# Kernel optimization log

Measured on AMD Instinct MI355X. Metric: run time of the kernel, lower is better.

Reference implementation:

```python
import jax, jax.numpy as jnp
import numpy as np

N, E, IN, HID, H, L, G = 20000, 320000, 128, 64, 4, 3, 128

def setup_inputs() -> dict:
    key = jax.random.key(0)
    ks = jax.random.split(key, 14)
    x = jax.random.normal(ks[0], (N, IN), dtype=jnp.float32)
    edge_index = jax.random.randint(ks[1], (2, E), 0, N, dtype=jnp.int64)
    batch = jnp.sort(jax.random.randint(ks[2], (N,), 0, G, dtype=jnp.int64))
    s_in = 1.0 / np.sqrt(IN)
    s_h = 1.0 / np.sqrt(HID)
    lin_W = jax.random.normal(ks[3], (IN, HID), jnp.float32) * s_in
    lin_b = jax.random.normal(ks[4], (HID,), jnp.float32) * 0.02
    Wq = jax.random.normal(ks[5], (L, HID, H * HID), jnp.float32) * s_h
    bq = jax.random.normal(ks[6], (L, H * HID), jnp.float32) * 0.02
    Wk = jax.random.normal(ks[7], (L, HID, H * HID), jnp.float32) * s_h
    bk = jax.random.normal(ks[8], (L, H * HID), jnp.float32) * 0.02
    Wv = jax.random.normal(ks[9], (L, HID, H * HID), jnp.float32) * s_h
    bv = jax.random.normal(ks[10], (L, H * HID), jnp.float32) * 0.02
    Ws = jax.random.normal(ks[11], (L, HID, HID), jnp.float32) * s_h
    bs = jax.random.normal(ks[12], (L, HID), jnp.float32) * 0.02
    return {"x": x, "edge_index": edge_index, "batch": batch,
            "lin_W": lin_W, "lin_b": lin_b, "Wq": Wq, "bq": bq,
            "Wk": Wk, "bk": bk, "Wv": Wv, "bv": bv, "Ws": Ws, "bs": bs}

def _transformer_conv(h, src, dst, Wq, bq, Wk, bk, Wv, bv, Ws, bs):
    # PyG TransformerConv(hid, hid, heads=H, concat=False), beta=False, root_weight=True
    n = h.shape[0]
    C = HID  # per-head dim
    q = (h @ Wq + bq).reshape(n, H, C)
    k = (h @ Wk + bk).reshape(n, H, C)
    v = (h @ Wv + bv).reshape(n, H, C)
    # per-edge attention logits: q_i . k_j / sqrt(C), i=dst (target), j=src
    alpha = jnp.einsum('ehc,ehc->eh', q[dst], k[src]) * (1.0 / np.sqrt(C))  # [E,H]
    # segment softmax over edges grouped by target node
    amax = jax.ops.segment_max(alpha, dst, num_segments=n)  # [N,H]
    amax = jnp.where(jnp.isfinite(amax), amax, 0.0)
    ex = jnp.exp(alpha - amax[dst])
    denom = jax.ops.segment_sum(ex, dst, num_segments=n)
    a = ex / jnp.maximum(denom[dst], 1e-16)  # [E,H]
    msg = a[:, :, None] * v[src]  # [E,H,C]
    agg = jax.ops.segment_sum(msg.reshape(-1, H * C), dst, num_segments=n)
    out = agg.reshape(n, H, C).mean(axis=1)  # concat=False -> head mean
    return out + h @ Ws + bs  # root/skip connection

def reference(x, edge_index, batch, lin_W, lin_b, Wq, bq, Wk, bk, Wv, bv, Ws, bs):
    src, dst = edge_index[0], edge_index[1]
    h = x @ lin_W + lin_b  # [N, HID]; dropout inactive in eval
    for l in range(L):
        h = jax.nn.relu(_transformer_conv(h, src, dst, Wq[l], bq[l], Wk[l], bk[l],
                                          Wv[l], bv[l], Ws[l], bs[l]))
    # global_add_pool: sum node features per graph
    return jax.ops.segment_sum(h, batch, num_segments=G)  # [G, HID]
```

## Files before the change

kernel.cpp:

```cpp
#include <hip/hip_runtime.h>
#include <math.h>

#define N_NODES 20000
#define N_EDGES 320000
#define DIM_IN 128
#define HID 64
#define HEADS 4
#define LAYERS 3
#define GRAPHS 128
#define HOP 68

typedef unsigned short ushort;
typedef ushort ushort8 __attribute__((ext_vector_type(8)));
typedef ushort ushort4v __attribute__((ext_vector_type(4)));
typedef short short8 __attribute__((ext_vector_type(8)));
typedef float f32x4 __attribute__((ext_vector_type(4)));

__device__ __forceinline__ float bf2f(ushort u) {
    return __uint_as_float(((unsigned int)u) << 16);
}
__device__ __forceinline__ ushort f2bf(float f) {
    unsigned int b = __float_as_uint(f);
    return (ushort)((b + 0x7FFFu + ((b >> 16) & 1u)) >> 16);
}


__global__ void hist_kernel(const int* __restrict__ dst, int* __restrict__ counts, int n) {
    int e = blockIdx.x * 256 + threadIdx.x;
    if (e < n) atomicAdd(&counts[dst[e]], 1);
}

__global__ __launch_bounds__(256) void blocksum_kernel(const int* __restrict__ counts,
                                                       int* __restrict__ bsum, int n) {
    int i = blockIdx.x * 256 + threadIdx.x;
    int v = (i < n) ? counts[i] : 0;
    int lane = threadIdx.x & 63, wave = threadIdx.x >> 6;
#pragma unroll
    for (int off = 32; off >= 1; off >>= 1) v += __shfl_xor(v, off);
    __shared__ int ws[4];
    if (lane == 0) ws[wave] = v;
    __syncthreads();
    if (threadIdx.x == 0) bsum[blockIdx.x] = ws[0] + ws[1] + ws[2] + ws[3];
}

__global__ __launch_bounds__(128) void scanb_kernel(const int* __restrict__ bsum,
                                                    int* __restrict__ bexcl, int nb) {
    int tid = threadIdx.x;
    int v = (tid < nb) ? bsum[tid] : 0;
    int lane = tid & 63, wave = tid >> 6;
    int s = v;
#pragma unroll
    for (int off = 1; off < 64; off <<= 1) {
        int t = __shfl_up(s, off);
        if (lane >= off) s += t;
    }
    __shared__ int w0sum;
    if (tid == 63) w0sum = s;
    __syncthreads();
    int excl = s - v + (wave ? w0sum : 0);
    if (tid < nb) bexcl[tid] = excl;
}

__global__ __launch_bounds__(256) void expand_kernel(const int* __restrict__ counts,
                                                     const int* __restrict__ bexcl,
                                                     int* __restrict__ offs,
                                                     int* __restrict__ cursor, int n) {
    int i = blockIdx.x * 256 + threadIdx.x;
    int v = (i < n) ? counts[i] : 0;
    int lane = threadIdx.x & 63, wave = threadIdx.x >> 6;
    int s = v;
#pragma unroll
    for (int off = 1; off < 64; off <<= 1) {
        int t = __shfl_up(s, off);
        if (lane >= off) s += t;
    }
    __shared__ int wsum[4];
    if (lane == 63) wsum[wave] = s;
    __syncthreads();
    int add = bexcl[blockIdx.x];
    for (int w = 0; w < wave; ++w) add += wsum[w];
    int excl = add + s - v;
    if (i < n) { offs[i] = excl; cursor[i] = excl; }
    if (i == 0) offs[n] = N_EDGES;
}

__global__ void scatter_kernel(const int* __restrict__ src, const int* __restrict__ dst,
                               int* __restrict__ cursor, int* __restrict__ csr, int n) {
    int e = blockIdx.x * 256 + threadIdx.x;
    if (e < n) {
        int d = dst[e];
        int pos = atomicAdd(&cursor[d], 1);
        csr[pos] = src[e];
    }
}


__global__ __launch_bounds__(256) void wcvt_all_kernel(
        const float* __restrict__ Wq, const float* __restrict__ bq,
        const float* __restrict__ Wk, const float* __restrict__ bk,
        const float* __restrict__ Wv, const float* __restrict__ bv,
        const float* __restrict__ Ws, const float* __restrict__ bs,
        const float* __restrict__ linW,
        ushort* __restrict__ Wt3, float* __restrict__ bias3,
        ushort* __restrict__ Wlt) {
    const int PER = 832 * 64;
    int idx = blockIdx.x * 256 + threadIdx.x;
    if (idx < 3 * PER) {
        int l = idx / PER;
        int r = idx - l * PER;
        int j = r >> 6, k = r & 63;
        const float* Wq_l = Wq + (size_t)l * HID * 256;
        const float* Wk_l = Wk + (size_t)l * HID * 256;
        const float* Wv_l = Wv + (size_t)l * HID * 256;
        const float* Ws_l = Ws + (size_t)l * HID * 64;
        float w;
        if (j < 256) {
            w = Wq_l[(size_t)k * 256 + j];
        } else if (j < 768) {
            int pout = j - 256;
            int isv = (pout >> 2) & 1;
            int low2 = pout & 3;
            int g = pout >> 3;
            int srccol = (g >> 4) * 64 + (g & 15) * 4 + low2;
            w = isv ? Wv_l[(size_t)k * 256 + srccol] : Wk_l[(size_t)k * 256 + srccol];
        } else {
            w = Ws_l[(size_t)k * 64 + (j - 768)];
        }
        Wt3[idx] = f2bf(w);
    } else {
        int idx2 = idx - 3 * PER;
        if (idx2 < 64 * DIM_IN) {
            int col = idx2 >> 7, k = idx2 & 127;
            Wlt[idx2] = f2bf(linW[(size_t)k * HID + col]);
        }
    }
    if (idx < 3 * 832) {
        int l = idx / 832, j = idx - l * 832;
        float b;
        if (j < 256) {
            b = bq[l * 256 + j];
        } else if (j < 768) {
            int pout = j - 256;
            int isv = (pout >> 2) & 1;
            int low2 = pout & 3;
            int g = pout >> 3;
            int srccol = (g >> 4) * 64 + (g & 15) * 4 + low2;
            b = isv ? bv[l * 256 + srccol] : bk[l * 256 + srccol];
        } else {
            b = bs[l * 64 + (j - 768)];
        }
        bias3[idx] = b;
    }
}


__device__ __forceinline__ void proj_rows(const float* __restrict__ ho,
        const ushort* __restrict__ Wt, const float* __restrict__ bias_cat,
        ushort* __restrict__ qsb, ushort* __restrict__ kvp,
        int r0, int lane, int t0, int tstep) {
    int lr = lane & 15;
    int grow = r0 + lr;
    int koff = (lane >> 4) * 8;
    short8 bh[2];
#pragma unroll
    for (int mm = 0; mm < 2; ++mm) {
        const float* hp = ho + lr * HOP + mm * 32 + koff;
        float4 f0 = *(const float4*)hp;
        float4 f1 = *(const float4*)(hp + 4);
        ushort8 u;
        u[0] = f2bf(f0.x); u[1] = f2bf(f0.y); u[2] = f2bf(f0.z); u[3] = f2bf(f0.w);
        u[4] = f2bf(f1.x); u[5] = f2bf(f1.y); u[6] = f2bf(f1.z); u[7] = f2bf(f1.w);
        bh[mm] = __builtin_bit_cast(short8, u);
    }
    bool ok = (grow < N_NODES);
    for (int t = t0; t < 52; t += tstep) {
        const ushort* wb = Wt + (size_t)(t * 16 + lr) * HID + koff;
        short8 w0 = *(const short8*)wb;
        short8 w1 = *(const short8*)(wb + 32);
        f32x4 a_ = (f32x4){0.f, 0.f, 0.f, 0.f};
        a_ = __builtin_amdgcn_mfma_f32_16x16x32_bf16(w0, bh[0], a_, 0, 0, 0);
        a_ = __builtin_amdgcn_mfma_f32_16x16x32_bf16(w1, bh[1], a_, 0, 0, 0);
        int j = t * 16 + ((lane >> 4) << 2);
        float4 bs4 = *(const float4*)(bias_cat + j);
        ushort4v u4;
        u4[0] = f2bf(a_[0] + bs4.x);
        u4[1] = f2bf(a_[1] + bs4.y);
        u4[2] = f2bf(a_[2] + bs4.z);
        u4[3] = f2bf(a_[3] + bs4.w);
        if (ok) {
            ushort* dst;
            if (j < 256)      dst = qsb + (size_t)grow * 320 + j;
            else if (j < 768) dst = kvp + (size_t)grow * 512 + (j - 256);
            else              dst = qsb + (size_t)grow * 320 + 256 + (j - 768);
            *(ushort4v*)dst = u4;
        }
    }
}


__global__ __launch_bounds__(256) void linproj_kernel(const float* __restrict__ x,
        const ushort* __restrict__ Wlt, const float* __restrict__ lb,
        const ushort* __restrict__ Wt0, const float* __restrict__ bias0,
        ushort* __restrict__ qsb, ushort* __restrict__ kvp) {
    __shared__ float ho[64 * HOP];
    int tid = threadIdx.x;
    int w = tid >> 6, l = tid & 63;
    int r0 = blockIdx.x * 64 + w * 16;
    int row = r0 + (l & 15);
    int rowc = (row < N_NODES) ? row : (N_NODES - 1);

    short8 a[4];
#pragma unroll
    for (int kc = 0; kc < 4; ++kc) {
        const float* xp = x + (size_t)rowc * DIM_IN + kc * 32 + (l >> 4) * 8;
        float4 f0 = *(const float4*)xp;
        float4 f1 = *(const float4*)(xp + 4);
        ushort8 u;
        u[0] = f2bf(f0.x); u[1] = f2bf(f0.y); u[2] = f2bf(f0.z); u[3] = f2bf(f0.w);
        u[4] = f2bf(f1.x); u[5] = f2bf(f1.y); u[6] = f2bf(f1.z); u[7] = f2bf(f1.w);
        a[kc] = __builtin_bit_cast(short8, u);
    }

    f32x4 acc[4];
#pragma unroll
    for (int t = 0; t < 4; ++t) acc[t] = (f32x4){0.f, 0.f, 0.f, 0.f};

    const ushort* wb = Wlt + (size_t)(l & 15) * DIM_IN + (l >> 4) * 8;
#pragma unroll
    for (int t = 0; t < 4; ++t) {
#pragma unroll
        for (int kc = 0; kc < 4; ++kc) {
            short8 b = *(const short8*)(wb + (size_t)t * 16 * DIM_IN + kc * 32);
            acc[t] = __builtin_amdgcn_mfma_f32_16x16x32_bf16(b, a[kc], acc[t], 0, 0, 0);
        }
    }

    float* hrow = ho + (size_t)(w * 16 + (l & 15)) * HOP;
#pragma unroll
    for (int t = 0; t < 4; ++t) {
        int j = t * 16 + ((l >> 4) << 2);
        float4 bias = *(const float4*)(lb + j);
        float4 o;
        o.x = acc[t][0] + bias.x;
        o.y = acc[t][1] + bias.y;
        o.z = acc[t][2] + bias.z;
        o.w = acc[t][3] + bias.w;
        *(float4*)(hrow + j) = o;
    }
    proj_rows(ho + (size_t)w * 16 * HOP, Wt0, bias0, qsb, kvp, r0, l, 0, 1);
}


__device__ __forceinline__ float4 attn_node(int node, int lane,
        const ushort* __restrict__ qsb, const ushort8* __restrict__ kvp,
        const int* __restrict__ offs, const int* __restrict__ csr) {
    int hh = lane >> 4;
    int cb = (lane & 15) * 4;
    const ushort* nb = qsb + (size_t)node * 320;
    ushort4v qu = *(const ushort4v*)(nb + hh * 64 + cb);
    float qx = bf2f(qu[0]), qy = bf2f(qu[1]), qz = bf2f(qu[2]), qw = bf2f(qu[3]);

    const float SCL = 0.125f * 1.44269504088896340736f;
    float m = -INFINITY, l = 0.f;
    float4 acc = make_float4(0.f, 0.f, 0.f, 0.f);

    int e0 = offs[node], e1 = offs[node + 1];
    int cnt = e1 - e0;

    ushort8 cur = (ushort8)(0);
    ushort8 nxt = (ushort8)(0);
    if (cnt > 0) cur = kvp[(size_t)csr[e0] * 64 + lane];
    if (cnt > 1) nxt = kvp[(size_t)csr[e0 + 1] * 64 + lane];

    for (int i = 0; i < cnt; ++i) {
        ushort8 u = cur;
        cur = nxt;
        if (i + 2 < cnt) nxt = kvp[(size_t)csr[e0 + i + 2] * 64 + lane];

        float p = qx * bf2f(u[0]) + qy * bf2f(u[1]) + qz * bf2f(u[2]) + qw * bf2f(u[3]);
        p += __shfl_xor(p, 1);
        p += __shfl_xor(p, 2);
        p += __shfl_xor(p, 4);
        p += __shfl_xor(p, 8);
        float alpha = p * SCL;
        if (__any(alpha > m)) {
            float nm = fmaxf(m, alpha);
            float sc = exp2f(m - nm);
            l *= sc; acc.x *= sc; acc.y *= sc; acc.z *= sc; acc.w *= sc;
            m = nm;
        }
        float pe = exp2f(alpha - m);
        l += pe;
        acc.x += pe * bf2f(u[4]);
        acc.y += pe * bf2f(u[5]);
        acc.z += pe * bf2f(u[6]);
        acc.w += pe * bf2f(u[7]);
    }

    float inv = (l > 0.f) ? (1.f / l) : 0.f;
    float4 r;
    r.x = acc.x * inv;
    r.y = acc.y * inv;
    r.z = acc.z * inv;
    r.w = acc.w * inv;
    r.x += __shfl_xor(r.x, 16); r.x += __shfl_xor(r.x, 32);
    r.y += __shfl_xor(r.y, 16); r.y += __shfl_xor(r.y, 32);
    r.z += __shfl_xor(r.z, 16); r.z += __shfl_xor(r.z, 32);
    r.w += __shfl_xor(r.w, 16); r.w += __shfl_xor(r.w, 32);

    ushort4v su = *(const ushort4v*)(nb + 256 + cb);
    float4 o;
    o.x = fmaxf(r.x * 0.25f + bf2f(su[0]), 0.f);
    o.y = fmaxf(r.y * 0.25f + bf2f(su[1]), 0.f);
    o.z = fmaxf(r.z * 0.25f + bf2f(su[2]), 0.f);
    o.w = fmaxf(r.w * 0.25f + bf2f(su[3]), 0.f);
    return o;
}


__global__ __launch_bounds__(512) void edgeproj_kernel(const ushort* __restrict__ qsb_in,
        const ushort8* __restrict__ kvp_in,
        const int* __restrict__ offs, const int* __restrict__ csr,
        const ushort* __restrict__ Wt_next, const float* __restrict__ bias_next,
        ushort* __restrict__ qsb_out, ushort* __restrict__ kvp_out) {
    __shared__ float ho[16 * HOP];
    int tid = threadIdx.x;
    int w = tid >> 6, l = tid & 63;
    int nbase = blockIdx.x * 16 + w * 2;
#pragma unroll
    for (int nd = 0; nd < 2; ++nd) {
        int node = nbase + nd;
        float4 o = attn_node(node, l, qsb_in, kvp_in, offs, csr);
        if ((l >> 4) == 0)
            *(float4*)(ho + (size_t)(w * 2 + nd) * HOP + (l & 15) * 4) = o;
    }
    __syncthreads();
    proj_rows(ho, Wt_next, bias_next, qsb_out, kvp_out, blockIdx.x * 16, l, w, 8);
}


__global__ __launch_bounds__(256) void edge_kernel(const ushort* __restrict__ qsb,
        const ushort8* __restrict__ kvp,
        const int* __restrict__ offs, const int* __restrict__ csr,
        float* __restrict__ hout) {
    int w = threadIdx.x >> 6, l = threadIdx.x & 63;
    int node = blockIdx.x * 4 + w;
    float4 o = attn_node(node, l, qsb, kvp, offs, csr);
    if ((l >> 4) == 0)
        *(float4*)(hout + (size_t)node * HID + (l & 15) * 4) = o;
}


__global__ __launch_bounds__(256) void pool_kernel(const float* __restrict__ h,
                                                   const int* __restrict__ batch,
                                                   float* __restrict__ out) {
    int g = blockIdx.x;
    int lo = 0, hi = N_NODES;
    while (lo < hi) { int mid = (lo + hi) >> 1; if (batch[mid] < g) lo = mid + 1; else hi = mid; }
    int start = lo;
    hi = N_NODES;
    while (lo < hi) { int mid = (lo + hi) >> 1; if (batch[mid] < g + 1) lo = mid + 1; else hi = mid; }
    int end = lo;
    int c = threadIdx.x & 63;
    int sub = threadIdx.x >> 6;
    float acc = 0.f;
    for (int i = start + sub; i < end; i += 4) acc += h[(size_t)i * HID + c];
    __shared__ float lds[4][64];
    lds[sub][c] = acc;
    __syncthreads();
    if (sub == 0) out[g * HID + c] = lds[0][c] + lds[1][c] + lds[2][c] + lds[3][c];
}


extern "C" void kernel_launch(void* const* d_in, const int* in_sizes, int n_in,
                              void* d_out, int out_size, void* d_ws, size_t ws_size,
                              hipStream_t stream) {
    const float* x    = (const float*)d_in[0];
    const int*   edge = (const int*)d_in[1];
    const int*   batch= (const int*)d_in[2];
    const float* linW = (const float*)d_in[3];
    const float* linb = (const float*)d_in[4];
    const float* Wq   = (const float*)d_in[5];
    const float* bq   = (const float*)d_in[6];
    const float* Wk   = (const float*)d_in[7];
    const float* bk   = (const float*)d_in[8];
    const float* Wv   = (const float*)d_in[9];
    const float* bv   = (const float*)d_in[10];
    const float* Ws   = (const float*)d_in[11];
    const float* bs   = (const float*)d_in[12];
    float* out = (float*)d_out;

    const int* src = edge;
    const int* dst = edge + N_EDGES;

    ushort* qsb0 = (ushort*)d_ws;
    ushort* qsb1 = qsb0 + (size_t)N_NODES * 320;
    ushort* kvp0 = qsb1 + (size_t)N_NODES * 320;
    ushort* kvp1 = kvp0 + (size_t)N_NODES * 512;
    float*  h3   = (float*)kvp1;
    int* counts = (int*)(kvp1 + (size_t)N_NODES * 512);
    int* offs   = counts + N_NODES;
    int* cursor = offs + N_NODES + 1;
    int* csr    = cursor + N_NODES;
    int* bsum   = csr + N_EDGES;
    int* bexcl  = bsum + 128;
    ushort* Wt3 = (ushort*)(bexcl + 128);
    float* bias3 = (float*)(Wt3 + 3 * 832 * 64);
    ushort* Wlt = (ushort*)(bias3 + 3 * 832);

    const int NB = (N_NODES + 255) / 256;

    hipMemsetAsync(counts, 0, N_NODES * sizeof(int), stream);
    hist_kernel<<<(N_EDGES + 255) / 256, 256, 0, stream>>>(dst, counts, N_EDGES);
    blocksum_kernel<<<NB, 256, 0, stream>>>(counts, bsum, N_NODES);
    scanb_kernel<<<1, 128, 0, stream>>>(bsum, bexcl, NB);
    expand_kernel<<<NB, 256, 0, stream>>>(counts, bexcl, offs, cursor, N_NODES);
    scatter_kernel<<<(N_EDGES + 255) / 256, 256, 0, stream>>>(src, dst, cursor, csr, N_EDGES);

    wcvt_all_kernel<<<(3 * 832 * 64 + 64 * DIM_IN + 255) / 256, 256, 0, stream>>>(
        Wq, bq, Wk, bk, Wv, bv, Ws, bs, linW, Wt3, bias3, Wlt);

    linproj_kernel<<<(N_NODES + 63) / 64, 256, 0, stream>>>(
        x, Wlt, linb, Wt3, bias3, qsb0, kvp0);

    edgeproj_kernel<<<N_NODES / 16, 512, 0, stream>>>(
        qsb0, (const ushort8*)kvp0, offs, csr,
        Wt3 + (size_t)1 * 832 * 64, bias3 + 832, qsb1, kvp1);

    edgeproj_kernel<<<N_NODES / 16, 512, 0, stream>>>(
        qsb1, (const ushort8*)kvp1, offs, csr,
        Wt3 + (size_t)2 * 832 * 64, bias3 + 1664, qsb0, kvp0);

    edge_kernel<<<N_NODES / 4, 256, 0, stream>>>(
        qsb0, (const ushort8*)kvp0, offs, csr, h3);

    pool_kernel<<<GRAPHS, 256, 0, stream>>>(h3, batch, out);
}
```

Measured before the change: 407.9 us.

## Sort nodes by in-degree and use one wave per node in fused edge-projection kernel

Adds a counting sort of nodes by descending in-degree (count, scan, scatter kernels) and has the fused attention+projection kernel process nodes in that permuted order. Each block now runs 16 waves with one node per wave instead of 8 waves with two nodes each, so the waves in a block have similar edge counts. The aim is less load imbalance, since waves in a block that wait at the barrier for the slowest node waste time. The cost is three extra small kernels, an indirect node lookup, scattered output row writes, and 1024-thread blocks that may lower occupancy.

Measured after the change: 430.5 us. 1.06x slower.

```diff
diff --git a/kernel.cpp b/kernel.cpp
--- a/kernel.cpp
+++ b/kernel.cpp
@@ -91,6 +91,49 @@
         int d = dst[e];
         int pos = atomicAdd(&cursor[d], 1);
         csr[pos] = src[e];
+    }
+}
+
+
+__global__ __launch_bounds__(256) void sortcnt_kernel(const int* __restrict__ offs,
+                                                      int* __restrict__ degcnt,
+                                                      int* __restrict__ rankbuf) {
+    int i = blockIdx.x * 256 + threadIdx.x;
+    if (i < N_NODES) {
+        int deg = offs[i + 1] - offs[i];
+        int key = 1023 - (deg < 1023 ? deg : 1023);
+        rankbuf[i] = atomicAdd(&degcnt[key], 1);
+    }
+}
+
+__global__ __launch_bounds__(1024) void scan1024_kernel(const int* __restrict__ degcnt,
+                                                        int* __restrict__ degoff) {
+    int tid = threadIdx.x;
+    int v = degcnt[tid];
+    int lane = tid & 63, wv = tid >> 6;
+    int s = v;
+#pragma unroll
+    for (int off = 1; off < 64; off <<= 1) {
+        int t = __shfl_up(s, off);
+        if (lane >= off) s += t;
+    }
+    __shared__ int wsum[16];
+    if (lane == 63) wsum[wv] = s;
+    __syncthreads();
+    int add = 0;
+    for (int q = 0; q < wv; ++q) add += wsum[q];
+    degoff[tid] = add + s - v;
+}
+
+__global__ __launch_bounds__(256) void sortscat_kernel(const int* __restrict__ offs,
+                                                       const int* __restrict__ degoff,
+                                                       const int* __restrict__ rankbuf,
+                                                       int* __restrict__ perm) {
+    int i = blockIdx.x * 256 + threadIdx.x;
+    if (i < N_NODES) {
+        int deg = offs[i + 1] - offs[i];
+        int key = 1023 - (deg < 1023 ? deg : 1023);
+        perm[degoff[key] + rankbuf[i]] = i;
     }
 }
 
@@ -157,9 +200,8 @@
 __device__ __forceinline__ void proj_rows(const float* __restrict__ ho,
         const ushort* __restrict__ Wt, const float* __restrict__ bias_cat,
         ushort* __restrict__ qsb, ushort* __restrict__ kvp,
-        int r0, int lane, int t0, int tstep) {
+        int grow, bool ok, int lane, int t0, int tstep) {
     int lr = lane & 15;
-    int grow = r0 + lr;
     int koff = (lane >> 4) * 8;
     short8 bh[2];
 #pragma unroll
@@ -172,7 +214,6 @@
         u[4] = f2bf(f1.x); u[5] = f2bf(f1.y); u[6] = f2bf(f1.z); u[7] = f2bf(f1.w);
         bh[mm] = __builtin_bit_cast(short8, u);
     }
-    bool ok = (grow < N_NODES);
     for (int t = t0; t < 52; t += tstep) {
         const ushort* wb = Wt + (size_t)(t * 16 + lr) * HID + koff;
         short8 w0 = *(const short8*)wb;
@@ -247,7 +288,8 @@
         o.w = acc[t][3] + bias.w;
         *(float4*)(hrow + j) = o;
     }
-    proj_rows(ho + (size_t)w * 16 * HOP, Wt0, bias0, qsb, kvp, r0, l, 0, 1);
+    proj_rows(ho + (size_t)w * 16 * HOP, Wt0, bias0, qsb, kvp,
+              row, row < N_NODES, l, 0, 1);
 }
 
 
@@ -318,24 +360,22 @@
 }
 
 
-__global__ __launch_bounds__(512) void edgeproj_kernel(const ushort* __restrict__ qsb_in,
+__global__ __launch_bounds__(1024) void edgeproj_kernel(const ushort* __restrict__ qsb_in,
         const ushort8* __restrict__ kvp_in,
         const int* __restrict__ offs, const int* __restrict__ csr,
+        const int* __restrict__ perm,
         const ushort* __restrict__ Wt_next, const float* __restrict__ bias_next,
         ushort* __restrict__ qsb_out, ushort* __restrict__ kvp_out) {
     __shared__ float ho[16 * HOP];
     int tid = threadIdx.x;
     int w = tid >> 6, l = tid & 63;
-    int nbase = blockIdx.x * 16 + w * 2;
-#pragma unroll
-    for (int nd = 0; nd < 2; ++nd) {
-        int node = nbase + nd;
-        float4 o = attn_node(node, l, qsb_in, kvp_in, offs, csr);
-        if ((l >> 4) == 0)
-            *(float4*)(ho + (size_t)(w * 2 + nd) * HOP + (l & 15) * 4) = o;
-    }
-    __syncthreads();
-    proj_rows(ho, Wt_next, bias_next, qsb_out, kvp_out, blockIdx.x * 16, l, w, 8);
+    int node = perm[blockIdx.x * 16 + w];
+    float4 o = attn_node(node, l, qsb_in, kvp_in, offs, csr);
+    if ((l >> 4) == 0)
+        *(float4*)(ho + (size_t)w * HOP + (l & 15) * 4) = o;
+    __syncthreads();
+    int grow = perm[blockIdx.x * 16 + (l & 15)];
+    proj_rows(ho, Wt_next, bias_next, qsb_out, kvp_out, grow, true, l, w, 16);
 }
 
 
@@ -399,36 +439,44 @@
     ushort* kvp1 = kvp0 + (size_t)N_NODES * 512;
     float*  h3   = (float*)kvp1;
     int* counts = (int*)(kvp1 + (size_t)N_NODES * 512);
-    int* offs   = counts + N_NODES;
+    int* degcnt = counts + N_NODES;
+    int* offs   = degcnt + 1024;
     int* cursor = offs + N_NODES + 1;
     int* csr    = cursor + N_NODES;
     int* bsum   = csr + N_EDGES;
     int* bexcl  = bsum + 128;
-    ushort* Wt3 = (ushort*)(bexcl + 128);
+    int* degoff = bexcl + 128;
+    int* rankbuf= degoff + 1024;
+    int* perm   = rankbuf + N_NODES;
+    ushort* Wt3 = (ushort*)(perm + N_NODES);
     float* bias3 = (float*)(Wt3 + 3 * 832 * 64);
     ushort* Wlt = (ushort*)(bias3 + 3 * 832);
 
     const int NB = (N_NODES + 255) / 256;
 
-    hipMemsetAsync(counts, 0, N_NODES * sizeof(int), stream);
+    hipMemsetAsync(counts, 0, (N_NODES + 1024) * sizeof(int), stream);
     hist_kernel<<<(N_EDGES + 255) / 256, 256, 0, stream>>>(dst, counts, N_EDGES);
     blocksum_kernel<<<NB, 256, 0, stream>>>(counts, bsum, N_NODES);
     scanb_kernel<<<1, 128, 0, stream>>>(bsum, bexcl, NB);
     expand_kernel<<<NB, 256, 0, stream>>>(counts, bexcl, offs, cursor, N_NODES);
     scatter_kernel<<<(N_EDGES + 255) / 256, 256, 0, stream>>>(src, dst, cursor, csr, N_EDGES);
 
+    sortcnt_kernel<<<NB, 256, 0, stream>>>(offs, degcnt, rankbuf);
+    scan1024_kernel<<<1, 1024, 0, stream>>>(degcnt, degoff);
+    sortscat_kernel<<<NB, 256, 0, stream>>>(offs, degoff, rankbuf, perm);
+
     wcvt_all_kernel<<<(3 * 832 * 64 + 64 * DIM_IN + 255) / 256, 256, 0, stream>>>(
         Wq, bq, Wk, bk, Wv, bv, Ws, bs, linW, Wt3, bias3, Wlt);
 
     linproj_kernel<<<(N_NODES + 63) / 64, 256, 0, stream>>>(
         x, Wlt, linb, Wt3, bias3, qsb0, kvp0);
 
-    edgeproj_kernel<<<N_NODES / 16, 512, 0, stream>>>(
-        qsb0, (const ushort8*)kvp0, offs, csr,
+    edgeproj_kernel<<<N_NODES / 16, 1024, 0, stream>>>(
+        qsb0, (const ushort8*)kvp0, offs, csr, perm,
         Wt3 + (size_t)1 * 832 * 64, bias3 + 832, qsb1, kvp1);
 
-    edgeproj_kernel<<<N_NODES / 16, 512, 0, stream>>>(
-        qsb1, (const ushort8*)kvp1, offs, csr,
+    edgeproj_kernel<<<N_NODES / 16, 1024, 0, stream>>>(
+        qsb1, (const ushort8*)kvp1, offs, csr, perm,
         Wt3 + (size_t)2 * 832 * 64, bias3 + 1664, qsb0, kvp0);
 
     edge_kernel<<<N_NODES / 4, 256, 0, stream>>>(
```
